# Optimization experiments

Measured on AMD Instinct MI355X. Metric: run time of the kernel, lower is better.

## Reference

```python
import jax, jax.numpy as jnp
import numpy as np

B, N, D, NH, L, DFF = 2, 2048, 256, 8, 4, 1024
DH = D // NH
FACTOR = 0.5 / float(np.sqrt(DH))  # == 1/sqrt(4*DH), matches q/k feature dim 4*d_head
EPS = 1e-5


def _ln(x, g, b):
    m = x.mean(-1, keepdims=True)
    v = ((x - m) ** 2).mean(-1, keepdims=True)
    return (x - m) * jax.lax.rsqrt(v + EPS) * g + b


def setup_inputs() -> dict:
    key = jax.random.key(0)
    ks = jax.random.split(key, 16)
    s = 0.05
    r = lambda i, shape: jax.random.normal(ks[i], shape, dtype=jnp.float32)
    return {
        "H": r(0, (B, N, D)),
        "V": r(1, (B, N, 3, D)),
        "D_batch": r(2, (B, N, N)),
        "rbf_feat": r(3, (L, B, 1, N, N)),
        "H_mask": jnp.ones((B, N), dtype=bool),
        "ln1_g": jnp.ones((L, D)), "ln1_b": jnp.zeros((L, D)),
        "ln2_g": jnp.ones((L, D)), "ln2_b": jnp.zeros((L, D)),
        "Wq": r(4, (L, D, 4 * D)) * s, "bq": jnp.zeros((L, 4 * D)),
        "Wk": r(5, (L, D, 4 * D)) * s, "bk": jnp.zeros((L, 4 * D)),
        "Wv": r(6, (L, D, D)) * s, "bv": jnp.zeros((L, D)),
        "Wvv": r(7, (L, D, D)) * s,
        "Wo": r(8, (L, D, D)) * s, "bo": jnp.zeros((L, D)),
        "Wvo": r(9, (L, D, D)) * s,
        "Wlv": r(10, (L, D, 2 * D)) * s,
        "W1": r(11, (L, 2 * D, DFF)) * s, "b1": jnp.zeros((L, DFF)),
        "W2": r(12, (L, DFF, 2 * D)) * s, "b2": jnp.zeros((L, 2 * D)),
    }


def _stack_forward(H, V, D_batch, rbf_feat, H_mask, ln1_g, ln1_b, ln2_g, ln2_b,
                   Wq, bq, Wk, bk, Wv, bv, Wvv, Wo, bo, Wvo, Wlv, W1, b1, W2, b2):
    b, n = H.shape[:2]
    mask = H_mask[:, None, None, :]       # [B,1,1,N] masks key columns
    base_bias = D_batch[:, None]          # [B,1,N,N]

    def step(carry, xs):
        H, V = carry
        (rbf, g1, be1, g2, be2, wq, bq_, wk, bk_, wv, bv_, wvv,
         wo, bo_, wvo, wlv, w1, b1_, w2, b2_) = xs
        # --- self-attention sublayer (pre-LN on scalar stream only) ---
        Hn = _ln(H, g1, be1)
        Hq = (Hn @ wq + bq_).reshape(b, n, NH, 4 * DH)
        Hk = (Hn @ wk + bk_).reshape(b, n, NH, 4 * DH)
        Hv = (Hn @ wv + bv_).reshape(b, n, NH, DH)
        Vv = (V @ wvv).reshape(b, n, 3, NH, DH)
        Vv = jnp.swapaxes(Vv, 2, 3).reshape(b, n, NH, 3 * DH)
        V_attn = jnp.concatenate([Hv, Vv], axis=-1)        # [B,N,H,4*DH]
        bias = jnp.where(mask, rbf + base_bias, -jnp.inf)  # [B,1,N,N]
        scores = jnp.einsum('bnhd,bmhd->bhnm', Hq, Hk) * FACTOR + bias
        attn = jax.nn.softmax(scores, axis=-1)
        res = jnp.einsum('bhnm,bmhd->bnhd', attn, V_attn)  # [B,N,H,4*DH]
        H_res = res[..., :DH].reshape(b, n, D)
        V_res = jnp.swapaxes(res[..., DH:].reshape(b, n, NH, 3, DH), 2, 3).reshape(b, n, 3, D)
        H = H + (H_res @ wo + bo_)
        V = V + V_res @ wvo
        # --- GVP FFN sublayer (pre-LN on scalar stream only) ---
        Hn = _ln(H, g2, be2)
        Vp = V @ wlv                                       # [B,N,3,2D]
        V1, V2 = Vp[..., :D], Vp[..., D:]
        scaler = jnp.concatenate([Hn, jnp.linalg.norm(V1, axis=-2)], axis=-1)
        sc = jax.nn.silu(scaler @ w1 + b1_) @ w2 + b2_
        H = H + sc[..., :D]
        V = V + sc[..., D:][..., None, :] * V2             # vector_act='none'
        return (H, V), None

    xs = (rbf_feat, ln1_g, ln1_b, ln2_g, ln2_b, Wq, bq, Wk, bk, Wv, bv, Wvv,
          Wo, bo, Wvo, Wlv, W1, b1, W2, b2)
    (H, V), _ = jax.lax.scan(step, (H, V), xs)
    return H, V


def reference(H, V, D_batch, rbf_feat, H_mask, ln1_g, ln1_b, ln2_g, ln2_b,
              Wq, bq, Wk, bk, Wv, bv, Wvv, Wo, bo, Wvo, Wlv, W1, b1, W2, b2):
    return _stack_forward(H, V, D_batch, rbf_feat, H_mask, ln1_g, ln1_b, ln2_g, ln2_b,
                          Wq, bq, Wk, bk, Wv, bv, Wvv, Wo, bo, Wvo, Wlv, W1, b1, W2, b2)
```

## Files before the change

kernel.cpp:

```cpp
#include <hip/hip_runtime.h>
#include <math.h>

static constexpr int B_  = 2;
static constexpr int N_  = 2048;
static constexpr int D_  = 256;
static constexpr int NH_ = 8;
static constexpr int L_  = 4;
static constexpr int DH_ = 32;
static constexpr int DQ_ = 128;
static constexpr float FACTOR_ = 0.08838834764831845f;
static constexpr float LOG2E_  = 1.4426950408889634f;
static constexpr float EPS_ = 1e-5f;

typedef short    short8   __attribute__((ext_vector_type(8)));
typedef unsigned short us4 __attribute__((ext_vector_type(4)));
typedef unsigned short us8 __attribute__((ext_vector_type(8)));
typedef float    f32x4    __attribute__((ext_vector_type(4)));
typedef unsigned short us;

__device__ __forceinline__ us f2b(float f) {
  unsigned u = __float_as_uint(f);
  unsigned r = u + 0x7FFF + ((u >> 16) & 1);
  return (us)(r >> 16);
}
__device__ __forceinline__ float b2f(us u) {
  return __uint_as_float(((unsigned)u) << 16);
}
__device__ __forceinline__ float e2(float x) {
  return __builtin_amdgcn_exp2f(x);
}
__device__ __forceinline__ void gl_lds16(const void* g, void* l) {
  __builtin_amdgcn_global_load_lds(
      (const __attribute__((address_space(1))) void*)g,
      (__attribute__((address_space(3))) void*)l, 16, 0, 0);
}

__global__ __launch_bounds__(256) void ln_kernel(const float* __restrict__ X,
    const float* __restrict__ g, const float* __restrict__ b,
    us* __restrict__ Y) {
  __shared__ float r1[256], r2[256];
  int row = blockIdx.x, tid = threadIdx.x;
  float x = X[(size_t)row * D_ + tid];
  r1[tid] = x; r2[tid] = x * x;
  __syncthreads();
  for (int s = 128; s > 0; s >>= 1) {
    if (tid < s) { r1[tid] += r1[tid + s]; r2[tid] += r2[tid + s]; }
    __syncthreads();
  }
  float mean = r1[0] * (1.0f / D_);
  float var  = r2[0] * (1.0f / D_) - mean * mean;
  float inv  = rsqrtf(var + EPS_);
  Y[(size_t)row * D_ + tid] = f2b((x - mean) * inv * g[tid] + b[tid]);
}

__global__ __launch_bounds__(256) void conv_bf16(const float* __restrict__ X,
    us* __restrict__ Y) {
  size_t i = ((size_t)blockIdx.x * 256 + threadIdx.x) * 4;
  float4 v = *(const float4*)&X[i];
  us4 o = { f2b(v.x), f2b(v.y), f2b(v.z), f2b(v.w) };
  *(us4*)&Y[i] = o;
}

__global__ __launch_bounds__(256) void biascomb(const float* __restrict__ R,
    const float* __restrict__ Dq, us* __restrict__ Out) {
  size_t i = ((size_t)blockIdx.x * 256 + threadIdx.x) * 8;
  float4 r0 = *(const float4*)&R[i];
  float4 r1 = *(const float4*)&R[i + 4];
  float4 d0 = *(const float4*)&Dq[i];
  float4 d1 = *(const float4*)&Dq[i + 4];
  us8 o = { f2b((r0.x + d0.x) * LOG2E_), f2b((r0.y + d0.y) * LOG2E_),
            f2b((r0.z + d0.z) * LOG2E_), f2b((r0.w + d0.w) * LOG2E_),
            f2b((r1.x + d1.x) * LOG2E_), f2b((r1.y + d1.y) * LOG2E_),
            f2b((r1.z + d1.z) * LOG2E_), f2b((r1.w + d1.w) * LOG2E_) };
  *(us8*)&Out[i] = o;
}

struct WConvDesc {
  const float* src[9];
  unsigned dst[9];
  int K[9];
  int N[9];
  int start[10];
};
__global__ __launch_bounds__(256) void wconv_kernel(WConvDesc d, us* __restrict__ Wb) {
  __shared__ float T[64][65];
  int bid = blockIdx.x, tid = threadIdx.x;
  int j = 0;
  #pragma unroll
  for (int q = 0; q < 8; q++) if (bid >= d.start[q + 1]) j = q + 1;
  int t = bid - d.start[j];
  int K = d.K[j], N = d.N[j];
  int tpr = N >> 6;
  int tk = t / tpr, tn = t - tk * tpr;
  const float* src = d.src[j];
  us* dst = Wb + d.dst[j];
  #pragma unroll
  for (int i = 0; i < 4; i++) {
    int r = i * 16 + (tid >> 4), c = (tid & 15) * 4;
    *(float4*)&T[r][c] = *(const float4*)&src[(size_t)(tk * 64 + r) * N + tn * 64 + c];
  }
  __syncthreads();
  #pragma unroll
  for (int i = 0; i < 4; i++) {
    int n = i * 16 + (tid >> 4), k = (tid & 15) * 4;
    us4 o = { f2b(T[k][n]), f2b(T[k + 1][n]), f2b(T[k + 2][n]), f2b(T[k + 3][n]) };
    *(us4*)&dst[(size_t)(tn * 64 + n) * K + tk * 64 + k] = o;
  }
}

template<int BM, int BN, int BIAS, int ACC, int SILU, int WF, int WB, int QKV, int MINW>
__global__ __launch_bounds__(256, MINW) void gemm_v2(const us* __restrict__ A,
    const us* __restrict__ Wt, const float* __restrict__ bias,
    const float* __restrict__ bias2, const float* __restrict__ bias3,
    float* __restrict__ Cf, us* __restrict__ Cb,
    int M, int K, int Nc, float oscale) {
  constexpr int NFM = BM / 32, NFN = BN / 32;
  constexpr int WSM = NFM * 16, WSN = NFN * 16;
  constexpr int NLA = BM / 32, NLB = BN / 32;
  __shared__ us As[2][BM * 64];
  __shared__ us Bs[2][BN * 64];
  const int tid = threadIdx.x;
  const int w = tid >> 6, l = tid & 63;
  const int lx = l & 15, ly = l >> 4;
  const int wr = w >> 1, wc = w & 1;
  const int bn = blockIdx.x, bm = blockIdx.y;
  const int swz = (lx & 7) << 4;
  const char* Ag = (const char*)A + (size_t)(bm * BM) * K * 2;
  const char* Bg = (const char*)Wt + (size_t)(bn * BN) * K * 2;
  const size_t rowb = (size_t)K * 2;

  #define GSTAGE(buf, k0)                                                     \
    do {                                                                      \
      _Pragma("unroll")                                                       \
      for (int j = 0; j < NLA; j++) {                                         \
        int o = j * 4096 + tid * 16;                                          \
        int r = o >> 7, cb = o & 127;                                         \
        int sc = cb ^ ((r & 7) << 4);                                         \
        gl_lds16(Ag + (size_t)r * rowb + (size_t)(k0) * 2 + sc,               \
                 &As[buf][(j * 4096 + w * 1024) >> 1]);                       \
      }                                                                       \
      _Pragma("unroll")                                                       \
      for (int j = 0; j < NLB; j++) {                                         \
        int o = j * 4096 + tid * 16;                                          \
        int r = o >> 7, cb = o & 127;                                         \
        int sc = cb ^ ((r & 7) << 4);                                         \
        gl_lds16(Bg + (size_t)r * rowb + (size_t)(k0) * 2 + sc,               \
                 &Bs[buf][(j * 4096 + w * 1024) >> 1]);                       \
      }                                                                       \
    } while (0)

  f32x4 acc[NFM][NFN];
  #pragma unroll
  for (int i = 0; i < NFM; i++)
    #pragma unroll
    for (int j = 0; j < NFN; j++) acc[i][j] = (f32x4){0.f, 0.f, 0.f, 0.f};

  int cur = 0;
  GSTAGE(0, 0);
  __syncthreads();
  for (int k0 = 0; k0 < K; k0 += 64) {
    if (k0 + 64 < K) GSTAGE(cur ^ 1, k0 + 64);
    #pragma unroll
    for (int s = 0; s < 2; s++) {
      short8 af[NFM], bf[NFN];
      #pragma unroll
      for (int mt = 0; mt < NFM; mt++)
        af[mt] = *(const short8*)
            &As[cur][(((wr * WSM + mt * 16 + lx) * 128) + ((s * 64 + ly * 16) ^ swz)) >> 1];
      #pragma unroll
      for (int nt = 0; nt < NFN; nt++)
        bf[nt] = *(const short8*)
            &Bs[cur][(((wc * WSN + nt * 16 + lx) * 128) + ((s * 64 + ly * 16) ^ swz)) >> 1];
      __builtin_amdgcn_s_setprio(1);
      #pragma unroll
      for (int mt = 0; mt < NFM; mt++)
        #pragma unroll
        for (int nt = 0; nt < NFN; nt++)
          acc[mt][nt] = __builtin_amdgcn_mfma_f32_16x16x32_bf16(af[mt], bf[nt], acc[mt][nt], 0, 0, 0);
      __builtin_amdgcn_s_setprio(0);
    }
    __syncthreads();
    cur ^= 1;
  }
  #undef GSTAGE

  #pragma unroll
  for (int nt = 0; nt < NFN; nt++) {
    const int n = bn * BN + wc * WSN + nt * 16 + lx;
    float bval = 0.f, osc = oscale;
    if (QKV) {
      if (n < 1024)      { bval = bias[n]; }
      else if (n < 2048) { bval = bias2[n - 1024]; osc = 1.0f; }
      else               { bval = bias3[n - 2048]; osc = 1.0f; }
    } else if (BIAS) {
      bval = bias[n];
    }
    #pragma unroll
    for (int mt = 0; mt < NFM; mt++) {
      #pragma unroll
      for (int r = 0; r < 4; r++) {
        const int m = bm * BM + wr * WSM + mt * 16 + ly * 4 + r;
        float v = acc[mt][nt][r] + bval;
        if (SILU) v = v / (1.f + __expf(-v));
        size_t idx = (size_t)m * Nc + n;
        if (ACC) v += Cf[idx];
        if (WF) Cf[idx] = v;
        if (WB) Cb[idx] = f2b(v * osc);
      }
    }
  }
}

__global__ __launch_bounds__(256, 3) void gemm_wo(const us* __restrict__ Hres,
    const us* __restrict__ Vres, const us* __restrict__ WtO,
    const us* __restrict__ WtVO, const float* __restrict__ bo,
    float* __restrict__ Hs, float* __restrict__ Vs, us* __restrict__ Vb) {
  constexpr int K = 256, Nc = 256;
  __shared__ us As[2][64 * 64];
  __shared__ us Bs[2][64 * 64];
  const int tid = threadIdx.x;
  const int w = tid >> 6, l = tid & 63;
  const int lx = l & 15, ly = l >> 4;
  const int wr = w >> 1, wc = w & 1;
  const int bn = blockIdx.x, bm = blockIdx.y;
  const bool isH = bm < 64;
  const int mb = isH ? bm : bm - 64;
  const int swz = (lx & 7) << 4;
  const char* Ag = (const char*)(isH ? Hres : Vres) + (size_t)(mb * 64) * K * 2;
  const char* Bg = (const char*)(isH ? WtO : WtVO) + (size_t)(bn * 64) * K * 2;
  const size_t rowb = (size_t)K * 2;

  #define GSTAGE(buf, k0)                                                     \
    do {                                                                      \
      _Pragma("unroll")                                                       \
      for (int j = 0; j < 2; j++) {                                           \
        int o = j * 4096 + tid * 16;                                          \
        int r = o >> 7, cb = o & 127;                                         \
        int sc = cb ^ ((r & 7) << 4);                                         \
        gl_lds16(Ag + (size_t)r * rowb + (size_t)(k0) * 2 + sc,               \
                 &As[buf][(j * 4096 + w * 1024) >> 1]);                       \
        gl_lds16(Bg + (size_t)r * rowb + (size_t)(k0) * 2 + sc,               \
                 &Bs[buf][(j * 4096 + w * 1024) >> 1]);                       \
      }                                                                       \
    } while (0)

  f32x4 acc[2][2];
  #pragma unroll
  for (int i = 0; i < 2; i++)
    #pragma unroll
    for (int j = 0; j < 2; j++) acc[i][j] = (f32x4){0.f, 0.f, 0.f, 0.f};

  int cur = 0;
  GSTAGE(0, 0);
  __syncthreads();
  for (int k0 = 0; k0 < K; k0 += 64) {
    if (k0 + 64 < K) GSTAGE(cur ^ 1, k0 + 64);
    #pragma unroll
    for (int s = 0; s < 2; s++) {
      short8 af[2], bf[2];
      #pragma unroll
      for (int mt = 0; mt < 2; mt++)
        af[mt] = *(const short8*)
            &As[cur][(((wr * 32 + mt * 16 + lx) * 128) + ((s * 64 + ly * 16) ^ swz)) >> 1];
      #pragma unroll
      for (int nt = 0; nt < 2; nt++)
        bf[nt] = *(const short8*)
            &Bs[cur][(((wc * 32 + nt * 16 + lx) * 128) + ((s * 64 + ly * 16) ^ swz)) >> 1];
      __builtin_amdgcn_s_setprio(1);
      #pragma unroll
      for (int mt = 0; mt < 2; mt++)
        #pragma unroll
        for (int nt = 0; nt < 2; nt++)
          acc[mt][nt] = __builtin_amdgcn_mfma_f32_16x16x32_bf16(af[mt], bf[nt], acc[mt][nt], 0, 0, 0);
      __builtin_amdgcn_s_setprio(0);
    }
    __syncthreads();
    cur ^= 1;
  }
  #undef GSTAGE

  #pragma unroll
  for (int nt = 0; nt < 2; nt++) {
    const int n = bn * 64 + wc * 32 + nt * 16 + lx;
    const float bval = isH ? bo[n] : 0.f;
    #pragma unroll
    for (int mt = 0; mt < 2; mt++) {
      #pragma unroll
      for (int r = 0; r < 4; r++) {
        const int m = mb * 64 + wr * 32 + mt * 16 + ly * 4 + r;
        size_t idx = (size_t)m * Nc + n;
        float v = acc[mt][nt][r] + bval;
        if (isH) {
          Hs[idx] += v;
        } else {
          float nv = Vs[idx] + v;
          Vs[idx] = nv;
          Vb[idx] = f2b(nv);
        }
      }
    }
  }
}

__global__ __launch_bounds__(256, 3) void gemm_w2(const us* __restrict__ A,
    const us* __restrict__ Wt, const float* __restrict__ b2,
    const float* __restrict__ Vp, float* __restrict__ Hs,
    float* __restrict__ Vs, us* __restrict__ Vb) {
  constexpr int K = 1024;
  __shared__ us As[2][64 * 64];
  __shared__ us Bs[2][64 * 64];
  const int tid = threadIdx.x;
  const int w = tid >> 6, l = tid & 63;
  const int lx = l & 15, ly = l >> 4;
  const int wr = w >> 1, wc = w & 1;
  const int bn = blockIdx.x, bm = blockIdx.y;
  const int swz = (lx & 7) << 4;
  const char* Ag = (const char*)A + (size_t)(bm * 64) * K * 2;
  const char* Bg = (const char*)Wt + (size_t)(bn * 64) * K * 2;
  const size_t rowb = (size_t)K * 2;

  #define GSTAGE(buf, k0)                                                     \
    do {                                                                      \
      _Pragma("unroll")                                                       \
      for (int j = 0; j < 2; j++) {                                           \
        int o = j * 4096 + tid * 16;                                          \
        int r = o >> 7, cb = o & 127;                                         \
        int sc = cb ^ ((r & 7) << 4);                                         \
        gl_lds16(Ag + (size_t)r * rowb + (size_t)(k0) * 2 + sc,               \
                 &As[buf][(j * 4096 + w * 1024) >> 1]);                       \
        gl_lds16(Bg + (size_t)r * rowb + (size_t)(k0) * 2 + sc,               \
                 &Bs[buf][(j * 4096 + w * 1024) >> 1]);                       \
      }                                                                      \
    } while (0)

  f32x4 acc[2][2];
  #pragma unroll
  for (int i = 0; i < 2; i++)
    #pragma unroll
    for (int j = 0; j < 2; j++) acc[i][j] = (f32x4){0.f, 0.f, 0.f, 0.f};

  int cur = 0;
  GSTAGE(0, 0);
  __syncthreads();
  for (int k0 = 0; k0 < K; k0 += 64) {
    if (k0 + 64 < K) GSTAGE(cur ^ 1, k0 + 64);
    #pragma unroll
    for (int s = 0; s < 2; s++) {
      short8 af[2], bf[2];
      #pragma unroll
      for (int mt = 0; mt < 2; mt++)
        af[mt] = *(const short8*)
            &As[cur][(((wr * 32 + mt * 16 + lx) * 128) + ((s * 64 + ly * 16) ^ swz)) >> 1];
      #pragma unroll
      for (int nt = 0; nt < 2; nt++)
        bf[nt] = *(const short8*)
            &Bs[cur][(((wc * 32 + nt * 16 + lx) * 128) + ((s * 64 + ly * 16) ^ swz)) >> 1];
      __builtin_amdgcn_s_setprio(1);
      #pragma unroll
      for (int mt = 0; mt < 2; mt++)
        #pragma unroll
        for (int nt = 0; nt < 2; nt++)
          acc[mt][nt] = __builtin_amdgcn_mfma_f32_16x16x32_bf16(af[mt], bf[nt], acc[mt][nt], 0, 0, 0);
      __builtin_amdgcn_s_setprio(0);
    }
    __syncthreads();
    cur ^= 1;
  }
  #undef GSTAGE

  const bool isH = (bn < 4);
  #pragma unroll
  for (int nt = 0; nt < 2; nt++) {
    const int n = bn * 64 + wc * 32 + nt * 16 + lx;
    const float bval = b2[n];
    #pragma unroll
    for (int mt = 0; mt < 2; mt++) {
      #pragma unroll
      for (int r = 0; r < 4; r++) {
        const int m = bm * 64 + wr * 32 + mt * 16 + ly * 4 + r;
        float v = acc[mt][nt][r] + bval;
        if (isH) {
          Hs[(size_t)m * D_ + n] += v;
        } else {
          const int j = n - 256;
          #pragma unroll
          for (int c = 0; c < 3; c++) {
            size_t vi = ((size_t)m * 3 + c) * D_ + j;
            float nv = Vs[vi] + v * Vp[((size_t)m * 3 + c) * 512 + 256 + j];
            Vs[vi] = nv;
            Vb[vi] = f2b(nv);
          }
        }
      }
    }
  }
}

__global__ __launch_bounds__(256) void pack_vattn_t(const us* __restrict__ QKVb,
    const us* __restrict__ Vv, us* __restrict__ Vt) {
  __shared__ us T[64][136];
  const int bid = blockIdx.x;
  const int nt = bid & 31, hh = (bid >> 5) & 7, b = bid >> 8;
  const int n0 = nt * 64;
  const int tid = threadIdx.x;
  {
    const int nn = tid >> 2, part = tid & 3;
    const size_t row = (size_t)(b * N_ + n0 + nn);
    const us* src = (part == 0) ? (QKVb + row * 2304 + 2048 + hh * DH_)
                                : (Vv + (row * 3 + (part - 1)) * D_ + hh * DH_);
    #pragma unroll
    for (int jj = 0; jj < 32; jj += 8)
      *(us8*)&T[nn][part * 32 + jj] = *(const us8*)(src + jj);
  }
  __syncthreads();
  const int d = tid >> 1, half = tid & 1;
  size_t ob = ((size_t)(b * NH_ + hh) * DQ_ + d) * (size_t)N_ + n0 + half * 32;
  #pragma unroll
  for (int i = 0; i < 32; i += 8) {
    us8 o;
    #pragma unroll
    for (int e = 0; e < 8; e++) o[e] = T[half * 32 + i + e][d];
    *(us8*)&Vt[ob + i] = o;
  }
}

__global__ __launch_bounds__(256, 3) void attn_mfma(
    const us* __restrict__ QKVb,
    const us* __restrict__ Vtb,
    const us* __restrict__ bias,
    us* __restrict__ Hres,
    us* __restrict__ Vres) {
  __shared__ us Kt[8192];
  __shared__ us Vt[8192];
  __shared__ us Plds[4][16][72];
  const int bid = blockIdx.x;
  const int h  = bid >> 6;
  const int g  = bid & 63;
  const int b  = g >> 5;
  const int qt = g & 31;
  const int tid = threadIdx.x;
  const int w  = tid >> 6;
  const int l  = tid & 63;
  const int lx = l & 15;
  const int ly = l >> 4;
  const int qrow = qt * 64 + w * 16 + lx;
  const int swz = (lx & 7) << 4;

  short8 qf[4];
  {
    const us* qp = QKVb + (size_t)(b * N_ + qrow) * 2304 + h * DQ_ + ly * 8;
    #pragma unroll
    for (int s = 0; s < 4; s++) qf[s] = *(const short8*)(qp + s * 32);
  }
  const char* kg = (const char*)QKVb + (size_t)b * N_ * 4608 + 2048 + h * 256;
  const char* vg = (const char*)(Vtb + ((size_t)(b * NH_ + h) * DQ_) * (size_t)N_);
  const us* bbase = bias + ((size_t)b * N_ + qrow) * N_;

  us8 kreg[4], vreg[4];
  #define LOADKV(m0)                                                          \
    do {                                                                      \
      _Pragma("unroll")                                                       \
      for (int j = 0; j < 4; j++) {                                           \
        int o = j * 4096 + tid * 16;                                          \
        int rk = o >> 8, ck = o & 255;                                        \
        kreg[j] = *(const us8*)(kg + (size_t)((m0) + rk) * 4608 +             \
                                (ck ^ ((rk & 7) << 4)));                      \
        int rv = o >> 7, cv = o & 127;                                        \
        vreg[j] = *(const us8*)(vg + (size_t)rv * (N_ * 2) +                  \
                                (size_t)(m0) * 2 + (cv ^ ((rv & 7) << 4)));   \
      }                                                                       \
    } while (0)
  #define WRITEKV()                                                           \
    do {                                                                      \
      _Pragma("unroll")                                                       \
      for (int j = 0; j < 4; j++) {                                           \
        *(us8*)&Kt[j * 2048 + tid * 8] = kreg[j];                             \
        *(us8*)&Vt[j * 2048 + tid * 8] = vreg[j];                             \
      }                                                                       \
    } while (0)

  float m_run = -3.0e38f, l_run = 0.f;
  f32x4 oacc[8];
  #pragma unroll
  for (int i = 0; i < 8; i++) oacc[i] = (f32x4){0.f, 0.f, 0.f, 0.f};

  LOADKV(0);
  WRITEKV();
  LOADKV(64);
  us4 bb[4];
  #pragma unroll
  for (int t = 0; t < 4; t++) bb[t] = *(const us4*)(bbase + t * 16 + ly * 4);
  __syncthreads();

  for (int mc0 = 0; mc0 < N_; mc0 += 64) {
    us4 bbn[4];
    if (mc0 + 64 < N_) {
      #pragma unroll
      for (int t = 0; t < 4; t++)
        bbn[t] = *(const us4*)(bbase + mc0 + 64 + t * 16 + ly * 4);
    }
    f32x4 sacc[4];
    #pragma unroll
    for (int t = 0; t < 4; t++) sacc[t] = (f32x4){0.f, 0.f, 0.f, 0.f};
    __builtin_amdgcn_s_setprio(1);
    #pragma unroll
    for (int t = 0; t < 4; t++) {
      #pragma unroll
      for (int s = 0; s < 4; s++) {
        const short8 kf = *(const short8*)
            &Kt[((t * 16 + lx) * 256 + ((s * 64 + ly * 16) ^ swz)) >> 1];
        sacc[t] = __builtin_amdgcn_mfma_f32_16x16x32_bf16(kf, qf[s], sacc[t], 0, 0, 0);
      }
    }
    __builtin_amdgcn_s_setprio(0);
    float pvv[16];
    #pragma unroll
    for (int t = 0; t < 4; t++) {
      pvv[t*4+0] = sacc[t][0] + b2f(bb[t][0]);
      pvv[t*4+1] = sacc[t][1] + b2f(bb[t][1]);
      pvv[t*4+2] = sacc[t][2] + b2f(bb[t][2]);
      pvv[t*4+3] = sacc[t][3] + b2f(bb[t][3]);
    }
    float a8[8], a4[4];
    #pragma unroll
    for (int i = 0; i < 8; i++) a8[i] = fmaxf(pvv[i], pvv[i + 8]);
    #pragma unroll
    for (int i = 0; i < 4; i++) a4[i] = fmaxf(a8[i], a8[i + 4]);
    float mloc = fmaxf(fmaxf(a4[0], a4[1]), fmaxf(a4[2], a4[3]));
    if (!__all(mloc - m_run <= 11.54f)) {
      mloc = fmaxf(mloc, __shfl_xor(mloc, 16, 64));
      mloc = fmaxf(mloc, __shfl_xor(mloc, 32, 64));
      float m_new = fmaxf(m_run, mloc);
      float scale = e2(m_run - m_new);
      l_run *= scale;
      #pragma unroll
      for (int i = 0; i < 8; i++) {
        oacc[i][0] *= scale; oacc[i][1] *= scale;
        oacc[i][2] *= scale; oacc[i][3] *= scale;
      }
      m_run = m_new;
    }
    float s8[8], s4[4];
    #pragma unroll
    for (int i = 0; i < 16; i++) pvv[i] = e2(pvv[i] - m_run);
    #pragma unroll
    for (int i = 0; i < 8; i++) s8[i] = pvv[i] + pvv[i + 8];
    #pragma unroll
    for (int i = 0; i < 4; i++) s4[i] = s8[i] + s8[i + 4];
    l_run += (s4[0] + s4[1]) + (s4[2] + s4[3]);
    #pragma unroll
    for (int t = 0; t < 4; t++) {
      us4 pk = { f2b(pvv[t*4+0]), f2b(pvv[t*4+1]), f2b(pvv[t*4+2]), f2b(pvv[t*4+3]) };
      *(us4*)&Plds[w][lx][t * 16 + ly * 4] = pk;
    }
    short8 pf0 = *(const short8*)&Plds[w][lx][ly * 8];
    short8 pf1 = *(const short8*)&Plds[w][lx][32 + ly * 8];
    __builtin_amdgcn_s_setprio(1);
    #pragma unroll
    for (int dt = 0; dt < 8; dt++) {
      const int rb = (dt * 16 + lx) * 128;
      const short8 vf0 = *(const short8*)&Vt[(rb + ((ly * 16) ^ swz)) >> 1];
      const short8 vf1 = *(const short8*)&Vt[(rb + ((64 + ly * 16) ^ swz)) >> 1];
      oacc[dt] = __builtin_amdgcn_mfma_f32_16x16x32_bf16(vf0, pf0, oacc[dt], 0, 0, 0);
      oacc[dt] = __builtin_amdgcn_mfma_f32_16x16x32_bf16(vf1, pf1, oacc[dt], 0, 0, 0);
    }
    __builtin_amdgcn_s_setprio(0);
    __syncthreads();
    if (mc0 + 64 < N_) {
      WRITEKV();
      if (mc0 + 128 < N_) LOADKV(mc0 + 128);
      #pragma unroll
      for (int t = 0; t < 4; t++) bb[t] = bbn[t];
      __syncthreads();
    }
  }
  #undef LOADKV
  #undef WRITEKV
  l_run += __shfl_xor(l_run, 16, 64);
  l_run += __shfl_xor(l_run, 32, 64);
  float inv = 1.0f / l_run;
  const size_t row = (size_t)(b * N_ + qrow);
  #pragma unroll
  for (int dt = 0; dt < 8; dt++) {
    const int d0 = dt * 16 + ly * 4;
    us4 pk = { f2b(oacc[dt][0] * inv), f2b(oacc[dt][1] * inv),
               f2b(oacc[dt][2] * inv), f2b(oacc[dt][3] * inv) };
    if (d0 < 32) {
      *(us4*)&Hres[row * D_ + h * DH_ + d0] = pk;
    } else {
      const int c = (d0 - DH_) >> 5, dd = (d0 - DH_) & 31;
      *(us4*)&Vres[(row * 3 + c) * D_ + h * DH_ + dd] = pk;
    }
  }
}

__global__ __launch_bounds__(256) void ln2scaler(const float* __restrict__ H,
    const float* __restrict__ g, const float* __restrict__ b,
    const float* __restrict__ Vp, us* __restrict__ scal) {
  __shared__ float r1[256], r2[256];
  size_t row = blockIdx.x;
  int j = threadIdx.x;
  float x = H[row * D_ + j];
  r1[j] = x; r2[j] = x * x;
  __syncthreads();
  for (int s = 128; s > 0; s >>= 1) {
    if (j < s) { r1[j] += r1[j + s]; r2[j] += r2[j + s]; }
    __syncthreads();
  }
  float mean = r1[0] * (1.0f / D_);
  float var  = r2[0] * (1.0f / D_) - mean * mean;
  float inv  = rsqrtf(var + EPS_);
  scal[row * 512 + j] = f2b((x - mean) * inv * g[j] + b[j]);
  float a  = Vp[(row * 3 + 0) * 512 + j];
  float c1 = Vp[(row * 3 + 1) * 512 + j];
  float c2 = Vp[(row * 3 + 2) * 512 + j];
  scal[row * 512 + D_ + j] = f2b(sqrtf(a * a + c1 * c1 + c2 * c2));
}

extern "C" void kernel_launch(void* const* d_in, const int* in_sizes, int n_in,
                              void* d_out, int out_size, void* d_ws, size_t ws_size,
                              hipStream_t stream) {
  const float* H_in = (const float*)d_in[0];
  const float* V_in = (const float*)d_in[1];
  const float* Db   = (const float*)d_in[2];
  const float* rbf  = (const float*)d_in[3];
  const float* ln1g = (const float*)d_in[5];
  const float* ln1b = (const float*)d_in[6];
  const float* ln2g = (const float*)d_in[7];
  const float* ln2b = (const float*)d_in[8];
  const float* Wq  = (const float*)d_in[9];
  const float* bq  = (const float*)d_in[10];
  const float* Wk  = (const float*)d_in[11];
  const float* bk  = (const float*)d_in[12];
  const float* Wv  = (const float*)d_in[13];
  const float* bv  = (const float*)d_in[14];
  const float* Wvv = (const float*)d_in[15];
  const float* Wo  = (const float*)d_in[16];
  const float* bo  = (const float*)d_in[17];
  const float* Wvo = (const float*)d_in[18];
  const float* Wlv = (const float*)d_in[19];
  const float* W1  = (const float*)d_in[20];
  const float* b1  = (const float*)d_in[21];
  const float* W2  = (const float*)d_in[22];
  const float* b2  = (const float*)d_in[23];

  const size_t HN = (size_t)B_ * N_ * D_;
  const size_t VN = HN * 3;
  float* Hs = (float*)d_out;
  float* Vs = (float*)d_out + HN;
  float* ws = (float*)d_ws;
  us*    bias_b = (us*)ws;
  us*    Wb     = (us*)(ws + 4194304);
  us*    Vb     = (us*)(ws + 5177344);
  us*    Hnb    = (us*)(ws + 6750208);
  us*    QKVb   = (us*)(ws + 7274496);
  us*    Vtb    = (us*)(ws + 11993088);
  us*    Vvb    = (us*)(ws + 14090240);
  us*    Hres_b = (us*)(ws + 6750208);
  us*    Vres_b = (us*)(ws + 14090240);
  float* Vp     = ws + 7274496;
  us*    scal_b = (us*)(ws + 13565952);
  us*    midb   = (us*)(ws + 15014528);

  hipMemcpyAsync(Hs, H_in, HN * sizeof(float), hipMemcpyDeviceToDevice, stream);
  hipMemcpyAsync(Vs, V_in, VN * sizeof(float), hipMemcpyDeviceToDevice, stream);
  conv_bf16<<<3072, 256, 0, stream>>>(V_in, Vb);

  const int ROWS  = B_ * N_;
  static const int wKs[9] = {256,256,256,256,256,256,256,512,1024};
  static const int wNs[9] = {1024,1024,256,256,256,256,512,1024,512};
  static const unsigned wOff[9] = {0,262144,524288,589824,655360,720896,786432,917504,1441792};
  static const int wStart[10] = {0,64,128,144,160,176,192,224,352,480};

  for (int l = 0; l < L_; ++l) {
    WConvDesc dsc;
    const float* srcs[9] = {
      Wq  + (size_t)l * 256 * 1024, Wk  + (size_t)l * 256 * 1024,
      Wv  + (size_t)l * 256 * 256,  Wvv + (size_t)l * 256 * 256,
      Wo  + (size_t)l * 256 * 256,  Wvo + (size_t)l * 256 * 256,
      Wlv + (size_t)l * 256 * 512,  W1  + (size_t)l * 512 * 1024,
      W2  + (size_t)l * 1024 * 512 };
    for (int j = 0; j < 9; j++) {
      dsc.src[j] = srcs[j]; dsc.dst[j] = wOff[j];
      dsc.K[j] = wKs[j]; dsc.N[j] = wNs[j]; dsc.start[j] = wStart[j];
    }
    dsc.start[9] = wStart[9];
    wconv_kernel<<<480, 256, 0, stream>>>(dsc, Wb);
    biascomb<<<4096, 256, 0, stream>>>(rbf + (size_t)l * B_ * N_ * N_, Db, bias_b);
    if (l == 0)
      ln_kernel<<<ROWS, 256, 0, stream>>>(Hs, ln1g, ln1b, Hnb);

    gemm_v2<128,64,0,0,0,0,1,1,3><<<dim3(36, 32), 256, 0, stream>>>(
        Hnb, Wb + wOff[0], bq + l * 1024, bk + l * 1024, bv + l * 256,
        nullptr, QKVb, 4096, 256, 2304, FACTOR_ * LOG2E_);
    gemm_v2<64,64,0,0,0,0,1,0,3><<<dim3(4, 192), 256, 0, stream>>>(
        Vb, Wb + wOff[3], nullptr, nullptr, nullptr, nullptr, Vvb, 12288, 256, 256, 1.f);
    pack_vattn_t<<<512, 256, 0, stream>>>(QKVb, Vvb, Vtb);
    attn_mfma<<<512, 256, 0, stream>>>(QKVb, Vtb, bias_b, Hres_b, Vres_b);
    gemm_wo<<<dim3(4, 256), 256, 0, stream>>>(
        Hres_b, Vres_b, Wb + wOff[4], Wb + wOff[5], bo + l * 256, Hs, Vs, Vb);
    gemm_v2<64,64,0,0,0,1,0,0,3><<<dim3(8, 192), 256, 0, stream>>>(
        Vb, Wb + wOff[6], nullptr, nullptr, nullptr, Vp, nullptr, 12288, 256, 512, 1.f);
    ln2scaler<<<ROWS, 256, 0, stream>>>(Hs, ln2g + l * D_, ln2b + l * D_, Vp, scal_b);
    gemm_v2<128,64,1,0,1,0,1,0,3><<<dim3(16, 32), 256, 0, stream>>>(
        scal_b, Wb + wOff[7], b1 + l * 1024, nullptr, nullptr, nullptr, midb, 4096, 512, 1024, 1.f);
    gemm_w2<<<dim3(8, 64), 256, 0, stream>>>(
        midb, Wb + wOff[8], b2 + l * 512, Vp, Hs, Vs, Vb);
    if (l < 3)
      ln_kernel<<<ROWS, 256, 0, stream>>>(Hs, ln1g + (l + 1) * D_,
                                          ln1b + (l + 1) * D_, Hnb);
  }
}
```

Measured before the change: 774.2 us.

## Split attention over key halves with separate log-sum-exp merge kernel

The attention kernel now splits the key dimension into two halves, launching twice as many blocks. Each block writes unnormalized fp32 partial outputs plus running max and sum to workspace. A new merge kernel rescales and combines the two halves, then writes the bf16 H and V residuals. This raises occupancy across the 256 CUs (512 blocks was only about two per CU), at the cost of extra fp32 traffic, a second kernel launch, and reloading Q per half.

```diff
diff --git a/kernel.cpp b/kernel.cpp
--- a/kernel.cpp
+++ b/kernel.cpp
@@ -428,16 +428,19 @@
     const us* __restrict__ QKVb,
     const us* __restrict__ Vtb,
     const us* __restrict__ bias,
-    us* __restrict__ Hres,
-    us* __restrict__ Vres) {
+    float* __restrict__ Of,
+    float* __restrict__ ml) {
   __shared__ us Kt[8192];
   __shared__ us Vt[8192];
   __shared__ us Plds[4][16][72];
   const int bid = blockIdx.x;
-  const int h  = bid >> 6;
-  const int g  = bid & 63;
+  const int half = bid >> 9;
+  const int sub = bid & 511;
+  const int h  = sub >> 6;
+  const int g  = sub & 63;
   const int b  = g >> 5;
   const int qt = g & 31;
+  const int mcbase = half * 1024;
   const int tid = threadIdx.x;
   const int w  = tid >> 6;
   const int l  = tid & 63;
@@ -484,17 +487,19 @@
   #pragma unroll
   for (int i = 0; i < 8; i++) oacc[i] = (f32x4){0.f, 0.f, 0.f, 0.f};
 
-  LOADKV(0);
+  LOADKV(mcbase);
   WRITEKV();
-  LOADKV(64);
+  LOADKV(mcbase + 64);
   us4 bb[4];
   #pragma unroll
-  for (int t = 0; t < 4; t++) bb[t] = *(const us4*)(bbase + t * 16 + ly * 4);
+  for (int t = 0; t < 4; t++)
+    bb[t] = *(const us4*)(bbase + mcbase + t * 16 + ly * 4);
   __syncthreads();
 
-  for (int mc0 = 0; mc0 < N_; mc0 += 64) {
+  const int mcend = mcbase + 1024;
+  for (int mc0 = mcbase; mc0 < mcend; mc0 += 64) {
     us4 bbn[4];
-    if (mc0 + 64 < N_) {
+    if (mc0 + 64 < mcend) {
       #pragma unroll
       for (int t = 0; t < 4; t++)
         bbn[t] = *(const us4*)(bbase + mc0 + 64 + t * 16 + ly * 4);
@@ -566,9 +571,9 @@
     }
     __builtin_amdgcn_s_setprio(0);
     __syncthreads();
-    if (mc0 + 64 < N_) {
+    if (mc0 + 64 < mcend) {
       WRITEKV();
-      if (mc0 + 128 < N_) LOADKV(mc0 + 128);
+      if (mc0 + 128 < mcend) LOADKV(mc0 + 128);
       #pragma unroll
       for (int t = 0; t < 4; t++) bb[t] = bbn[t];
       __syncthreads();
@@ -578,19 +583,39 @@
   #undef WRITEKV
   l_run += __shfl_xor(l_run, 16, 64);
   l_run += __shfl_xor(l_run, 32, 64);
-  float inv = 1.0f / l_run;
-  const size_t row = (size_t)(b * N_ + qrow);
-  #pragma unroll
-  for (int dt = 0; dt < 8; dt++) {
-    const int d0 = dt * 16 + ly * 4;
-    us4 pk = { f2b(oacc[dt][0] * inv), f2b(oacc[dt][1] * inv),
-               f2b(oacc[dt][2] * inv), f2b(oacc[dt][3] * inv) };
-    if (d0 < 32) {
-      *(us4*)&Hres[row * D_ + h * DH_ + d0] = pk;
-    } else {
-      const int c = (d0 - DH_) >> 5, dd = (d0 - DH_) & 31;
-      *(us4*)&Vres[(row * 3 + c) * D_ + h * DH_ + dd] = pk;
-    }
+  const int unit = (b * N_ + qrow) * NH_ + h;
+  const size_t ob = ((size_t)half * 32768 + unit) * 128;
+  #pragma unroll
+  for (int dt = 0; dt < 8; dt++)
+    *(f32x4*)&Of[ob + dt * 16 + ly * 4] = oacc[dt];
+  if (ly == 0) {
+    ml[((size_t)half * 32768 + unit) * 2 + 0] = m_run;
+    ml[((size_t)half * 32768 + unit) * 2 + 1] = l_run;
+  }
+}
+
+__global__ __launch_bounds__(256) void attn_merge(const float* __restrict__ Of,
+    const float* __restrict__ ml, us* __restrict__ Hres, us* __restrict__ Vres) {
+  const int unit = blockIdx.x * 8 + (threadIdx.x >> 5);
+  const int lane = threadIdx.x & 31;
+  const int rowG = unit >> 3, h = unit & 7;
+  const float m1 = ml[(size_t)unit * 2], l1 = ml[(size_t)unit * 2 + 1];
+  const float m2 = ml[(size_t)(32768 + unit) * 2], l2 = ml[(size_t)(32768 + unit) * 2 + 1];
+  const float m = fmaxf(m1, m2);
+  const float s1 = e2(m1 - m), s2 = e2(m2 - m);
+  const float inv = 1.0f / (l1 * s1 + l2 * s2);
+  const int d0 = lane * 4;
+  f32x4 o1 = *(const f32x4*)&Of[(size_t)unit * 128 + d0];
+  f32x4 o2 = *(const f32x4*)&Of[(size_t)(32768 + unit) * 128 + d0];
+  us4 pk = { f2b((o1[0] * s1 + o2[0] * s2) * inv),
+             f2b((o1[1] * s1 + o2[1] * s2) * inv),
+             f2b((o1[2] * s1 + o2[2] * s2) * inv),
+             f2b((o1[3] * s1 + o2[3] * s2) * inv) };
+  if (d0 < 32) {
+    *(us4*)&Hres[(size_t)rowG * D_ + h * DH_ + d0] = pk;
+  } else {
+    const int c = (d0 - DH_) >> 5, dd = (d0 - DH_) & 31;
+    *(us4*)&Vres[((size_t)rowG * 3 + c) * D_ + h * DH_ + dd] = pk;
   }
 }
 
@@ -661,6 +686,8 @@
   float* Vp     = ws + 7274496;
   us*    scal_b = (us*)(ws + 13565952);
   us*    midb   = (us*)(ws + 15014528);
+  float* Of     = ws + 17111680;
+  float* ml     = ws + 25500288;
 
   hipMemcpyAsync(Hs, H_in, HN * sizeof(float), hipMemcpyDeviceToDevice, stream);
   hipMemcpyAsync(Vs, V_in, VN * sizeof(float), hipMemcpyDeviceToDevice, stream);
@@ -696,7 +723,8 @@
     gemm_v2<64,64,0,0,0,0,1,0,3><<<dim3(4, 192), 256, 0, stream>>>(
         Vb, Wb + wOff[3], nullptr, nullptr, nullptr, nullptr, Vvb, 12288, 256, 256, 1.f);
     pack_vattn_t<<<512, 256, 0, stream>>>(QKVb, Vvb, Vtb);
-    attn_mfma<<<512, 256, 0, stream>>>(QKVb, Vtb, bias_b, Hres_b, Vres_b);
+    attn_mfma<<<1024, 256, 0, stream>>>(QKVb, Vtb, bias_b, Of, ml);
+    attn_merge<<<4096, 256, 0, stream>>>(Of, ml, Hres_b, Vres_b);
     gemm_wo<<<dim3(4, 256), 256, 0, stream>>>(
         Hres_b, Vres_b, Wb + wOff[4], Wb + wOff[5], bo + l * 256, Hs, Vs, Vb);
     gemm_v2<64,64,0,0,0,1,0,0,3><<<dim3(8, 192), 256, 0, stream>>>(
```

After: 841.5 us. 8.7% more time.
